# Kernel tuning notes

Measured on AMD Instinct MI355X. Metric: run time of the kernel, lower is better.

## Reference

```python
import jax, jax.numpy as jnp
import numpy as np

NEG_SLOPE = 0.01  # LeakyReLU default
STRIDE = 5        # group_length // 4
EPS = 1e-5        # RMSNorm eps


def leaky_relu(x):
    return jnp.where(x >= 0, x, NEG_SLOPE * x)


def rmsnorm(x, w):
    return x * jax.lax.rsqrt(jnp.mean(x * x, axis=-1, keepdims=True) + EPS) * w


def s6(x, fc1_w, fc1_b, fc2_w, fc2_b, fc3_w, fc3_b, A):
    # x: [B, L, D] with D = 2*d_model; A: [D, N]
    delta = jax.nn.softplus(x @ fc1_w.T + fc1_b)        # [B, L, D]
    Bm = x @ fc2_w.T + fc2_b                             # [B, L, N]
    Cm = x @ fc3_w.T + fc3_b                             # [B, L, N]
    dA = jnp.exp(jnp.einsum('bld,dn->bldn', delta, A))   # [B, L, D, N]
    dBx = jnp.einsum('bld,bln,bld->bldn', delta, Bm, x)  # delta * B * x

    def step(h, inp):
        dA_t, dBx_t = inp
        h = dA_t * h + dBx_t
        return h, h

    B_, L, D, N = dA.shape
    h0 = jnp.zeros((B_, D, N), dtype=x.dtype)
    _, hs = jax.lax.scan(step, h0, (jnp.swapaxes(dA, 0, 1), jnp.swapaxes(dBx, 0, 1)))
    hs = jnp.swapaxes(hs, 0, 1)                          # [B, L, D, N]
    return jnp.einsum('bln,bldn->bld', Cm, hs)           # [B, L, D]


def setup_inputs() -> dict:
    key = jax.random.key(0)
    ks = iter(jax.random.split(key, 32))

    def rn(shape, scale=0.02):
        return scale * jax.random.normal(next(ks), shape, dtype=jnp.float32)

    B, band, gl, d, N, L = 256, 189, 20, 128, 128, 34
    di = 2 * d
    return {
        'x': jax.random.normal(next(ks), (B, 1, band), dtype=jnp.float32),
        'conv_w': rn((d, 1, gl)), 'conv_b': rn((d,)),
        'norm_w': jnp.ones((d,), jnp.float32),
        'inp_w': rn((di, d)), 'inp_b': rn((di,)),
        'seqconv_w': rn((L, L, 3)), 'seqconv_b': rn((L,)),
        'convlin_w': rn((di, di)), 'convlin_b': rn((di,)),
        'fc1_w': rn((di, di)), 'fc1_b': rn((di,)),
        'fc2_w': rn((N, di)), 'fc2_b': rn((N,)),
        'fc3_w': rn((N, di)), 'fc3_b': rn((N,)),
        'A': jnp.ones((di, N), jnp.float32) / jnp.sqrt(jnp.float32(N)),
        'D_w': rn((di, d)), 'D_b': rn((di,)),
        'out_w': rn((d, di)), 'out_b': rn((d,)),
        'fnn1_w': rn((64, L * d)), 'fnn1_b': rn((64,)),
        'fnn2_w': rn((32, 64)), 'fnn2_b': rn((32,)),
    }


def reference(x, conv_w, conv_b, norm_w, inp_w, inp_b, seqconv_w, seqconv_b,
              convlin_w, convlin_b, fc1_w, fc1_b, fc2_w, fc2_b, fc3_w, fc3_b,
              A, D_w, D_b, out_w, out_b, fnn1_w, fnn1_b, fnn2_w, fnn2_b):
    # group division: Conv1d(1, d, k=20, stride=5) + LeakyReLU
    g = jax.lax.conv_general_dilated(x, conv_w, (STRIDE,), [(0, 0)],
                                     dimension_numbers=('NCH', 'OIH', 'NCH'))
    g = leaky_relu(g + conv_b[None, :, None])            # [B, d, L]
    h = jnp.swapaxes(g, 1, 2)                            # [B, L, d]
    # Mamba block
    xn = rmsnorm(h, norm_w)
    xp = xn @ inp_w.T + inp_b                            # [B, L, 2d]
    # Conv1d(seq_len, seq_len, k=3, pad=1): seq axis L is the channel dim
    xc = jax.lax.conv_general_dilated(xp, seqconv_w, (1,), [(1, 1)],
                                      dimension_numbers=('NCH', 'OIH', 'NCH'))
    xc = jax.nn.silu(xc + seqconv_b[None, :, None])
    xc = xc @ convlin_w.T + convlin_b                    # [B, L, 2d]
    xs = s6(xc, fc1_w, fc1_b, fc2_w, fc2_b, fc3_w, fc3_b, A)
    y = jax.nn.silu(xs) * jax.nn.silu(xn @ D_w.T + D_b)  # gated
    y = y @ out_w.T + out_b                              # [B, L, d]
    # FNN head
    f = y.reshape(y.shape[0], -1)                        # [B, L*d]
    f = leaky_relu(f @ fnn1_w.T + fnn1_b)
    return f @ fnn2_w.T + fnn2_b                         # [B, 32]
```

## Files before the change

kernel.cpp:

```cpp
#include <hip/hip_runtime.h>
#include <math.h>


#define NB    256
#define LL    34
#define DD    128
#define DI    256
#define NN    128
#define MM    (NB*LL)

using u16 = unsigned short;
typedef __attribute__((ext_vector_type(8))) short short8;
typedef __attribute__((ext_vector_type(4))) float f32x4;

__device__ __forceinline__ float silu_f(float x)  { return x / (1.f + __expf(-x)); }
__device__ __forceinline__ float softplus_f(float x) {
    return fmaxf(x, 0.f) + __logf(1.f + __expf(-fabsf(x)));
}
__device__ __forceinline__ float leaky_f(float x) { return (x >= 0.f) ? x : 0.01f * x; }

__device__ __forceinline__ u16 f2bf(float x) {
    unsigned u = __float_as_uint(x);
    return (u16)((u + 0x7FFF + ((u >> 16) & 1)) >> 16);
}
__device__ __forceinline__ float bf2f(u16 h) {
    return __uint_as_float(((unsigned)h) << 16);
}
__device__ __forceinline__ void f2pair(float v, u16* h, u16* l) {
    u16 hh = f2bf(v);
    *h = hh;
    *l = f2bf(v - bf2f(hh));
}

__global__ __launch_bounds__(256)
void prep_conv_k(const float* __restrict__ x, const float* __restrict__ cw,
                 const float* __restrict__ cb, const float* __restrict__ nw,
                 u16* __restrict__ XNh, u16* __restrict__ XNl,
                 const float* __restrict__ inp_w, const float* __restrict__ D_w,
                 const float* __restrict__ fc1_w, const float* __restrict__ fc2_w,
                 const float* __restrict__ fc3_w, const float* __restrict__ convlin_w,
                 const float* __restrict__ out_w,
                 const float* __restrict__ inp_b, const float* __restrict__ D_b,
                 const float* __restrict__ fc1_b, const float* __restrict__ fc2_b,
                 const float* __restrict__ fc3_b,
                 const float* __restrict__ W1, const float* __restrict__ A,
                 u16* __restrict__ wc1h, u16* __restrict__ wc1l,
                 u16* __restrict__ wc3h, u16* __restrict__ wc3l,
                 u16* __restrict__ cvh,  u16* __restrict__ cvl,
                 u16* __restrict__ owh,  u16* __restrict__ owl,
                 float* __restrict__ bias1, float* __restrict__ bias3,
                 float* __restrict__ W1T, int* __restrict__ flag)
{
    const int bx  = blockIdx.x;
    const int tid = threadIdx.x;
    __shared__ float tile[64][65];
    __shared__ float wsum[4];

    if (bx < 4352) {
        const int row = tid >> 7;
        const int c   = tid & 127;
        const int bl  = bx * 2 + row;
        const int b   = bl / LL, l = bl % LL;
        const float* xr = x + (size_t)b * 189 + l * 5;
        float g = cb[c];
        #pragma unroll
        for (int k = 0; k < 20; k++) g = fmaf(xr[k], cw[c * 20 + k], g);
        g = leaky_f(g);

        float s = g * g;
        #pragma unroll
        for (int m = 32; m >= 1; m >>= 1) s += __shfl_xor(s, m);
        if ((tid & 63) == 0) wsum[tid >> 6] = s;
        __syncthreads();
        float mean = (wsum[row * 2] + wsum[row * 2 + 1]) * (1.f / 128.f);
        float inv = 1.f / sqrtf(mean + 1e-5f);
        float v = g * inv * nw[c];
        f2pair(v, &XNh[(size_t)bl * DD + c], &XNl[(size_t)bl * DD + c]);
    } else if (bx < 5504) {
        int i = (bx - 4352) * 256 + tid;
        if (i < 65536) {
            float v = (i < 32768) ? inp_w[i] : D_w[i - 32768];
            f2pair(v, &wc1h[i], &wc1l[i]);
        } else if (i < 196608) {
            int j = i - 65536;
            float v = (j < 65536) ? fc1_w[j] : (j < 98304 ? fc2_w[j - 65536] : fc3_w[j - 98304]);
            f2pair(v, &wc3h[j], &wc3l[j]);
        } else if (i < 262144) {
            int j = i - 196608;
            f2pair(convlin_w[j], &cvh[j], &cvl[j]);
        } else if (i < 294912) {
            int j = i - 262144;
            f2pair(out_w[j], &owh[j], &owl[j]);
        }
        if (i < 512)  bias1[i] = (i < 256) ? inp_b[i] : D_b[i - 256];
        else if (i < 1024) {
            int j = i - 512;
            bias3[j] = (j < 256) ? fc1_b[j] : (j < 384 ? fc2_b[j - 256] : fc3_b[j - 384]);
        }
    } else if (bx < 5572) {
        const int bt = bx - 5504;
        for (int p = 0; p < 16; p++) {
            int idx = tid + p * 256;
            int r = idx >> 6, c = idx & 63;
            tile[r][c] = W1[(size_t)r * 4352 + bt * 64 + c];
        }
        __syncthreads();
        for (int p = 0; p < 16; p++) {
            int idx = tid + p * 256;
            int cc = idx >> 6, rr = idx & 63;
            W1T[(size_t)(bt * 64 + cc) * 64 + rr] = tile[rr][cc];
        }
    } else {
        __shared__ int s;
        if (tid == 0) s = 1;
        __syncthreads();
        bool ok = true;
        for (int k = 0; k < 128; k++) {
            int idx = tid + k * 256;
            ok &= (A[idx] == A[idx & ~127]);
        }
        if (!ok) s = 0;
        __syncthreads();
        if (tid == 0) *flag = s;
    }
}

template <int K, int EPI>
__global__ __launch_bounds__(256)
void mgemm_k(const u16* __restrict__ Ah, const u16* __restrict__ Al,
             const u16* __restrict__ Wh, const u16* __restrict__ Wl,
             const float* __restrict__ bias,
             float* __restrict__ Y, int ldy,
             u16* __restrict__ Yh, u16* __restrict__ Yl,
             u16* __restrict__ BC)
{
    const int tid  = threadIdx.x;
    const int r0   = blockIdx.x * 128;
    const int c0   = blockIdx.y * 64;
    const int wave = tid >> 6;
    const int lane = tid & 63;
    const int wm   = wave & 1;
    const int wn   = wave >> 1;
    const int l15  = lane & 15;
    const int lq   = lane >> 4;

    __shared__ u16 sAh[128][40];
    __shared__ u16 sAl[128][40];
    __shared__ u16 sBh[64][40];
    __shared__ u16 sBl[64][40];

    f32x4 acc[4][2];
    #pragma unroll
    for (int i = 0; i < 4; i++)
        #pragma unroll
        for (int j = 0; j < 2; j++) acc[i][j] = (f32x4){0.f, 0.f, 0.f, 0.f};

    const int a_row = tid >> 1;
    const int a_kb  = (tid & 1) * 16;
    const int b_row = tid >> 2;
    const int b_ko  = (tid & 3) * 8;

    for (int k0 = 0; k0 < K; k0 += 32) {
        const u16* ga = Ah + (size_t)(r0 + a_row) * K + k0 + a_kb;
        const u16* gl = Al + (size_t)(r0 + a_row) * K + k0 + a_kb;
        short8 vh0 = *(const short8*)(ga);
        short8 vh1 = *(const short8*)(ga + 8);
        short8 vl0 = *(const short8*)(gl);
        short8 vl1 = *(const short8*)(gl + 8);
        const u16* gb = Wh + (size_t)(c0 + b_row) * K + k0 + b_ko;
        const u16* gc = Wl + (size_t)(c0 + b_row) * K + k0 + b_ko;
        short8 wb = *(const short8*)(gb);
        short8 wc = *(const short8*)(gc);

        *(short8*)&sAh[a_row][a_kb]     = vh0;
        *(short8*)&sAh[a_row][a_kb + 8] = vh1;
        *(short8*)&sAl[a_row][a_kb]     = vl0;
        *(short8*)&sAl[a_row][a_kb + 8] = vl1;
        *(short8*)&sBh[b_row][b_ko] = wb;
        *(short8*)&sBl[b_row][b_ko] = wc;
        __syncthreads();

        short8 fah[4], fal[4], fbh[2], fbl[2];
        #pragma unroll
        for (int i = 0; i < 4; i++) {
            fah[i] = *(const short8*)&sAh[wm * 64 + i * 16 + l15][lq * 8];
            fal[i] = *(const short8*)&sAl[wm * 64 + i * 16 + l15][lq * 8];
        }
        #pragma unroll
        for (int j = 0; j < 2; j++) {
            fbh[j] = *(const short8*)&sBh[wn * 32 + j * 16 + l15][lq * 8];
            fbl[j] = *(const short8*)&sBl[wn * 32 + j * 16 + l15][lq * 8];
        }
        #pragma unroll
        for (int i = 0; i < 4; i++)
            #pragma unroll
            for (int j = 0; j < 2; j++) {
                acc[i][j] = __builtin_amdgcn_mfma_f32_16x16x32_bf16(fah[i], fbh[j], acc[i][j], 0, 0, 0);
                acc[i][j] = __builtin_amdgcn_mfma_f32_16x16x32_bf16(fah[i], fbl[j], acc[i][j], 0, 0, 0);
                acc[i][j] = __builtin_amdgcn_mfma_f32_16x16x32_bf16(fal[i], fbh[j], acc[i][j], 0, 0, 0);
            }
        __syncthreads();
    }

    #pragma unroll
    for (int i = 0; i < 4; i++) {
        int gr = r0 + wm * 64 + i * 16 + lq * 4;
        #pragma unroll
        for (int j = 0; j < 2; j++) {
            int gc = c0 + wn * 32 + j * 16 + l15;
            float bb = bias[gc];
            #pragma unroll
            for (int r = 0; r < 4; r++) {
                float v = acc[i][j][r] + bb;
                if (EPI == 1 || EPI == 3) { if (gc < 256) v = softplus_f(v); }
                if (EPI == 2) {
                    u16 hh, ll;
                    f2pair(v, &hh, &ll);
                    Yh[(size_t)(gr + r) * ldy + gc] = hh;
                    Yl[(size_t)(gr + r) * ldy + gc] = ll;
                } else {
                    Y[(size_t)(gr + r) * ldy + gc] = v;
                    if (EPI == 3 && gc >= 256) {
                        u16 hh, ll;
                        f2pair(v, &hh, &ll);
                        u16* rb = BC + (size_t)(gr + r) * 1024
                                     + ((gc < 384) ? 0 : 256) + (gc & 127);
                        rb[0]   = hh;
                        rb[128] = ll;
                    }
                }
            }
        }
    }
}

__global__ __launch_bounds__(256)
void seqconv_k(const float* __restrict__ XP, int ldxp,
               const float* __restrict__ w, const float* __restrict__ bias,
               u16* __restrict__ XCh, u16* __restrict__ XCl)
{
    const int b   = blockIdx.x;
    const int tid = threadIdx.x;
    const int tx  = tid & 63;
    const int ty  = tid >> 6;
    const int j0  = tx * 4;

    __shared__ float sx[LL][264];
    __shared__ float sw[LL][112];

    for (int idx = tid; idx < LL * 256; idx += 256) {
        int li = idx >> 8, jj = idx & 255;
        sx[li][jj + 1] = XP[(size_t)(b * LL + li) * ldxp + jj];
    }
    if (tid < LL) { sx[tid][0] = 0.f; sx[tid][257] = 0.f; }
    for (int idx = tid; idx < LL * LL * 3; idx += 256) {
        int lo = idx / 102;
        int rem = idx - lo * 102;
        int li = rem / 3;
        int k  = rem - li * 3;
        sw[li][lo * 3 + k] = w[idx];
    }
    __syncthreads();

    const int base = ty * 9 - (ty == 3 ? 1 : 0);
    const int cnt  = (ty < 2) ? 9 : 8;

    float acc[9][4];
    #pragma unroll
    for (int i = 0; i < 9; i++)
        #pragma unroll
        for (int jj = 0; jj < 4; jj++) acc[i][jj] = 0.f;

    for (int li = 0; li < LL; li++) {
        float4 xa = *(const float4*)&sx[li][j0];
        float2 xb = *(const float2*)&sx[li][j0 + 4];
        float xv[6] = {xa.x, xa.y, xa.z, xa.w, xb.x, xb.y};
        const float* swr = &sw[li][0];
        #pragma unroll
        for (int i = 0; i < 9; i++) {
            if (i < cnt) {
                int lo3 = (base + i) * 3;
                float w0 = swr[lo3 + 0];
                float w1 = swr[lo3 + 1];
                float w2 = swr[lo3 + 2];
                #pragma unroll
                for (int jj = 0; jj < 4; jj++) {
                    acc[i][jj] = fmaf(w0, xv[jj],     acc[i][jj]);
                    acc[i][jj] = fmaf(w1, xv[jj + 1], acc[i][jj]);
                    acc[i][jj] = fmaf(w2, xv[jj + 2], acc[i][jj]);
                }
            }
        }
    }

    #pragma unroll
    for (int i = 0; i < 9; i++) {
        if (i < cnt) {
            int lo = base + i;
            float bb = bias[lo];
            ushort4 oh, ol;
            float v0 = silu_f(acc[i][0] + bb);
            float v1 = silu_f(acc[i][1] + bb);
            float v2 = silu_f(acc[i][2] + bb);
            float v3 = silu_f(acc[i][3] + bb);
            f2pair(v0, &oh.x, &ol.x);
            f2pair(v1, &oh.y, &ol.y);
            f2pair(v2, &oh.z, &ol.z);
            f2pair(v3, &oh.w, &ol.w);
            size_t o = (size_t)(b * LL + lo) * DI + j0;
            *(ushort4*)&XCh[o] = oh;
            *(ushort4*)&XCl[o] = ol;
        }
    }
}

__global__ __launch_bounds__(256)
void scan_fb_k(const int* __restrict__ flag,
               const float* __restrict__ dBC,
               const u16*  __restrict__ Xh, const u16* __restrict__ Xl,
               const float* __restrict__ A,
               const float* __restrict__ DG,
               u16* __restrict__ Gh, u16* __restrict__ Gl)
{
    if (*flag != 0) return;
    const int b  = blockIdx.y;
    const int d0 = blockIdx.x * 64;
    const int tid = threadIdx.x;
    const int sub = tid & 15;
    const int pg  = tid >> 4;
    const int dbase = d0 + pg * 4;
    const int nA = sub * 4;

    float a[4][8], h[4][8];
    #pragma unroll
    for (int dd = 0; dd < 4; dd++) {
        const float* Ar = A + (size_t)(dbase + dd) * NN;
        float4 q0 = *(const float4*)(Ar + nA);
        float4 q1 = *(const float4*)(Ar + 64 + nA);
        a[dd][0]=q0.x; a[dd][1]=q0.y; a[dd][2]=q0.z; a[dd][3]=q0.w;
        a[dd][4]=q1.x; a[dd][5]=q1.y; a[dd][6]=q1.z; a[dd][7]=q1.w;
        #pragma unroll
        for (int j = 0; j < 8; j++) h[dd][j] = 0.f;
    }

    const float* pD  = dBC + (size_t)b * LL * 512 + dbase;
    const float* pBC = dBC + (size_t)b * LL * 512 + 256 + nA;
    const u16*  pXh = Xh  + (size_t)b * LL * 256 + dbase;
    const u16*  pXl = Xl  + (size_t)b * LL * 256 + dbase;
    const float* pG  = DG  + (size_t)b * LL * 512 + 256 + dbase;
    u16* pGh = Gh + (size_t)b * LL * 256 + dbase;
    u16* pGl = Gl + (size_t)b * LL * 256 + dbase;

    for (int l = 0; l < LL; l++) {
        float4  cD  = *(const float4*)(pD);
        ushort4 cXh = *(const ushort4*)(pXh);
        ushort4 cXl = *(const ushort4*)(pXl);
        float4 cB0 = *(const float4*)(pBC);
        float4 cB1 = *(const float4*)(pBC + 64);
        float4 cC0 = *(const float4*)(pBC + 128);
        float4 cC1 = *(const float4*)(pBC + 192);
        pD += 512; pBC += 512; pXh += 256; pXl += 256;

        float xv[4] = { bf2f(cXh.x) + bf2f(cXl.x), bf2f(cXh.y) + bf2f(cXl.y),
                        bf2f(cXh.z) + bf2f(cXl.z), bf2f(cXh.w) + bf2f(cXl.w) };
        float dl[4] = {cD.x, cD.y, cD.z, cD.w};
        float dx[4] = {cD.x * xv[0], cD.y * xv[1], cD.z * xv[2], cD.w * xv[3]};
        float bv[8] = {cB0.x,cB0.y,cB0.z,cB0.w,cB1.x,cB1.y,cB1.z,cB1.w};
        float cv[8] = {cC0.x,cC0.y,cC0.z,cC0.w,cC1.x,cC1.y,cC1.z,cC1.w};

        float accd[4] = {0.f, 0.f, 0.f, 0.f};
        #pragma unroll
        for (int dd = 0; dd < 4; dd++)
            #pragma unroll
            for (int j = 0; j < 8; j++) {
                float dA = __expf(dl[dd] * a[dd][j]);
                h[dd][j] = fmaf(dA, h[dd][j], dx[dd] * bv[j]);
                accd[dd] = fmaf(cv[j], h[dd][j], accd[dd]);
            }
        #pragma unroll
        for (int dd = 0; dd < 4; dd++) {
            float v = accd[dd];
            v += __shfl_xor(v, 1);
            v += __shfl_xor(v, 2);
            v += __shfl_xor(v, 4);
            v += __shfl_xor(v, 8);
            accd[dd] = v;
        }
        if (sub == 0) {
            float4 dg = *(const float4*)(pG);
            ushort4 oh, ol;
            float g0 = silu_f(accd[0]) * silu_f(dg.x);
            float g1 = silu_f(accd[1]) * silu_f(dg.y);
            float g2 = silu_f(accd[2]) * silu_f(dg.z);
            float g3 = silu_f(accd[3]) * silu_f(dg.w);
            f2pair(g0, &oh.x, &ol.x);
            f2pair(g1, &oh.y, &ol.y);
            f2pair(g2, &oh.z, &ol.z);
            f2pair(g3, &oh.w, &ol.w);
            *(ushort4*)pGh = oh;
            *(ushort4*)pGl = ol;
        }
        pG += 512; pGh += 256; pGl += 256;
    }
}

__global__ __launch_bounds__(512)
void ssd_tail_k(const int* __restrict__ flag,
                const float* __restrict__ dBC,
                const u16* __restrict__ BCp,
                const u16* __restrict__ Xh, const u16* __restrict__ Xl,
                const float* __restrict__ A,
                const float* __restrict__ DG,
                const u16* __restrict__ gFh, const u16* __restrict__ gFl,
                const u16* __restrict__ owh, const u16* __restrict__ owl,
                const float* __restrict__ outb,
                const float* __restrict__ W1T, const float* __restrict__ B1,
                const float* __restrict__ W2, const float* __restrict__ B2,
                float* __restrict__ out)
{
    const int b    = blockIdx.x;
    const int tid  = threadIdx.x;
    const int wave = tid >> 6;
    const int lane = tid & 63;
    const int l15  = lane & 15;
    const int lq   = lane >> 4;

    __shared__ __align__(16) char smem[71936];
    u16  (*sBh)[136] = (u16 (*)[136])(smem);
    u16  (*sBl)[136] = (u16 (*)[136])(smem + 13056);
    u16  (*sCh)[136] = (u16 (*)[136])(smem + 26112);
    u16  (*sCl)[136] = (u16 (*)[136])(smem + 39168);
    float (*sM)[49]  = (float (*)[49])(smem + 52224);
    u16  (*sGh)[264] = (u16 (*)[264])(smem);
    u16  (*sGl)[264] = (u16 (*)[264])(smem + 25344);
    float* sF        = (float*)(smem + 52224);
    float* s1p       = (float*)(smem + 69632);
    float* s1        = (float*)(smem + 71680);

    const bool uni = (*flag != 0);
    if (uni) {
        const u16* base = BCp + (size_t)b * LL * 1024;
        for (int idx = tid; idx < LL * 16; idx += 512) {
            int l = idx >> 4, c = (idx & 15) << 3;
            const u16* row = base + l * 1024;
            *(short8*)&sBh[l][c] = *(const short8*)&row[c];
            *(short8*)&sBl[l][c] = *(const short8*)&row[128 + c];
            *(short8*)&sCh[l][c] = *(const short8*)&row[256 + c];
            *(short8*)&sCl[l][c] = *(const short8*)&row[384 + c];
        }
        __syncthreads();

        for (int tt = wave; tt < 9; tt += 8) {
            int ti = tt / 3, tj = tt - ti * 3;
            f32x4 acc = (f32x4){0.f, 0.f, 0.f, 0.f};
            #pragma unroll
            for (int ks = 0; ks < 4; ks++) {
                short8 ch = *(const short8*)&sCh[ti * 16 + l15][ks * 32 + lq * 8];
                short8 cl = *(const short8*)&sCl[ti * 16 + l15][ks * 32 + lq * 8];
                short8 bh = *(const short8*)&sBh[tj * 16 + l15][ks * 32 + lq * 8];
                short8 bl = *(const short8*)&sBl[tj * 16 + l15][ks * 32 + lq * 8];
                acc = __builtin_amdgcn_mfma_f32_16x16x32_bf16(ch, bh, acc, 0, 0, 0);
                acc = __builtin_amdgcn_mfma_f32_16x16x32_bf16(ch, bl, acc, 0, 0, 0);
                acc = __builtin_amdgcn_mfma_f32_16x16x32_bf16(cl, bh, acc, 0, 0, 0);
            }
            #pragma unroll
            for (int r = 0; r < 4; r++)
                sM[ti * 16 + lq * 4 + r][tj * 16 + l15] = acc[r];
        }
        __syncthreads();

        if (tid < 256) {
            const int d = tid;
            const float a_d = A[(size_t)d * NN];
            const float* pDel = dBC + (size_t)b * LL * 512 + d;
            const u16* pXh = Xh + (size_t)b * LL * 256 + d;
            const u16* pXl = Xl + (size_t)b * LL * 256 + d;

            float u[LL], eS[LL];
            float S = 0.f;
            #pragma unroll
            for (int l = 0; l < LL; l++) {
                float dl = pDel[l * 512];
                S = fmaf(dl, a_d, S);
                eS[l] = __expf(S);
                float xv = bf2f(pXh[l * 256]) + bf2f(pXl[l * 256]);
                u[l] = __expf(-S) * dl * xv;
            }

            const float* pG = DG + (size_t)b * LL * 512 + 256 + d;
            #pragma unroll
            for (int l = 0; l < LL; l++) {
                float acc = 0.f;
                for (int t = 0; t <= l; t++) acc = fmaf(sM[l][t], u[t], acc);
                float xs = eS[l] * acc;
                float g = silu_f(xs) * silu_f(pG[l * 512]);
                u16 hh, ll2;
                f2pair(g, &hh, &ll2);
                sGh[l][d] = hh;
                sGl[l][d] = ll2;
            }
        } else {
            u16* zh = &sGh[34][0];
            u16* zl = &sGl[34][0];
            for (int idx = tid - 256; idx < 14 * 264; idx += 256) {
                zh[idx] = 0;
                zl[idx] = 0;
            }
        }
        __syncthreads();
    } else {
        for (int idx = tid; idx < LL * 32; idx += 512) {
            int l = idx >> 5, c = (idx & 31) << 3;
            *(short8*)&sGh[l][c] = *(const short8*)&gFh[((size_t)b * LL + l) * 256 + c];
            *(short8*)&sGl[l][c] = *(const short8*)&gFl[((size_t)b * LL + l) * 256 + c];
        }
        u16* zh = &sGh[34][0];
        u16* zl = &sGl[34][0];
        for (int idx = tid; idx < 14 * 264; idx += 512) {
            zh[idx] = 0;
            zl[idx] = 0;
        }
        __syncthreads();
    }

    {
        const int j0 = wave;
        f32x4 acc[3];
        #pragma unroll
        for (int i = 0; i < 3; i++) acc[i] = (f32x4){0.f, 0.f, 0.f, 0.f};
        #pragma unroll
        for (int ks = 0; ks < 8; ks++) {
            const size_t wo = (size_t)(j0 * 16 + l15) * 256 + ks * 32 + lq * 8;
            short8 bh = *(const short8*)&owh[wo];
            short8 bl = *(const short8*)&owl[wo];
            #pragma unroll
            for (int i = 0; i < 3; i++) {
                short8 ah = *(const short8*)&sGh[i * 16 + l15][ks * 32 + lq * 8];
                short8 al = *(const short8*)&sGl[i * 16 + l15][ks * 32 + lq * 8];
                acc[i] = __builtin_amdgcn_mfma_f32_16x16x32_bf16(ah, bh, acc[i], 0, 0, 0);
                acc[i] = __builtin_amdgcn_mfma_f32_16x16x32_bf16(ah, bl, acc[i], 0, 0, 0);
                acc[i] = __builtin_amdgcn_mfma_f32_16x16x32_bf16(al, bh, acc[i], 0, 0, 0);
            }
        }
        __syncthreads();
        #pragma unroll
        for (int i = 0; i < 3; i++) {
            int row = i * 16 + lq * 4;
            int col = j0 * 16 + l15;
            float bb = outb[col];
            #pragma unroll
            for (int r = 0; r < 4; r++)
                if (row + r < LL) sF[(row + r) * 128 + col] = acc[i][r] + bb;
        }
    }
    __syncthreads();

    {
        const int o = tid & 63;
        const int q = tid >> 6;
        const float* wp = W1T + ((size_t)q * 544) * 64 + o;
        const float* fp = sF + q * 544;
        float accf = 0.f;
        for (int k = 0; k < 544; k += 4) {
            float w0 = wp[(size_t)(k + 0) * 64];
            float w1 = wp[(size_t)(k + 1) * 64];
            float w2 = wp[(size_t)(k + 2) * 64];
            float w3 = wp[(size_t)(k + 3) * 64];
            accf = fmaf(w0, fp[k + 0], accf);
            accf = fmaf(w1, fp[k + 1], accf);
            accf = fmaf(w2, fp[k + 2], accf);
            accf = fmaf(w3, fp[k + 3], accf);
        }
        s1p[q * 64 + o] = accf;
    }
    __syncthreads();

    if (tid < 64) {
        float a0 = B1[tid];
        #pragma unroll
        for (int q = 0; q < 8; q++) a0 += s1p[q * 64 + tid];
        s1[tid] = leaky_f(a0);
    }
    __syncthreads();

    if (tid < 32) {
        float a2 = B2[tid];
        const float* w2 = W2 + tid * 64;
        #pragma unroll
        for (int j = 0; j < 64; j++) a2 = fmaf(s1[j], w2[j], a2);
        out[(size_t)b * 32 + tid] = a2;
    }
}

extern "C" void kernel_launch(void* const* d_in, const int* in_sizes, int n_in,
                              void* d_out, int out_size, void* d_ws, size_t ws_size,
                              hipStream_t stream)
{
    const float* x        = (const float*)d_in[0];
    const float* conv_w   = (const float*)d_in[1];
    const float* conv_b   = (const float*)d_in[2];
    const float* norm_w   = (const float*)d_in[3];
    const float* inp_w    = (const float*)d_in[4];
    const float* inp_b    = (const float*)d_in[5];
    const float* seqconv_w= (const float*)d_in[6];
    const float* seqconv_b= (const float*)d_in[7];
    const float* convlin_w= (const float*)d_in[8];
    const float* convlin_b= (const float*)d_in[9];
    const float* fc1_w    = (const float*)d_in[10];
    const float* fc1_b    = (const float*)d_in[11];
    const float* fc2_w    = (const float*)d_in[12];
    const float* fc2_b    = (const float*)d_in[13];
    const float* fc3_w    = (const float*)d_in[14];
    const float* fc3_b    = (const float*)d_in[15];
    const float* A        = (const float*)d_in[16];
    const float* D_w      = (const float*)d_in[17];
    const float* D_b      = (const float*)d_in[18];
    const float* out_w    = (const float*)d_in[19];
    const float* out_b    = (const float*)d_in[20];
    const float* fnn1_w   = (const float*)d_in[21];
    const float* fnn1_b   = (const float*)d_in[22];
    const float* fnn2_w   = (const float*)d_in[23];
    const float* fnn2_b   = (const float*)d_in[24];

    char* W = (char*)d_ws;
    float* buf1  = (float*)(W + 0);
    float* buf3  = (float*)(W + 17825792);
    u16*   xnh   = (u16*)  (W + 35651584);
    u16*   xnl   = (u16*)  (W + 37879808);
    u16*   xc2h  = (u16*)  (W + 35651584);
    u16*   xc2l  = (u16*)  (W + 40108032);
    u16*   xch   = (u16*)  (W + 44564480);
    u16*   xcl   = (u16*)  (W + 49020928);
    float* w1t   = (float*)(W + 53477376);
    u16*   wc1h  = (u16*)  (W + 54591488);
    u16*   wc1l  = (u16*)  (W + 54722560);
    u16*   wc3h  = (u16*)  (W + 54853632);
    u16*   wc3l  = (u16*)  (W + 55115776);
    u16*   cvh   = (u16*)  (W + 55377920);
    u16*   cvl   = (u16*)  (W + 55508992);
    u16*   owh   = (u16*)  (W + 55640064);
    u16*   owl   = (u16*)  (W + 55705600);
    float* bias1 = (float*)(W + 55771136);
    float* bias3 = (float*)(W + 55773184);
    int*   uflag = (int*)  (W + 55775232);
    u16* gateh = xch;
    u16* gatel = xcl;
    u16* bcpair = (u16*)buf1;

    prep_conv_k<<<5573, 256, 0, stream>>>(x, conv_w, conv_b, norm_w, xnh, xnl,
                                          inp_w, D_w, fc1_w, fc2_w, fc3_w,
                                          convlin_w, out_w,
                                          inp_b, D_b, fc1_b, fc2_b, fc3_b,
                                          fnn1_w, A,
                                          wc1h, wc1l, wc3h, wc3l, cvh, cvl,
                                          owh, owl, bias1, bias3, w1t, uflag);

    mgemm_k<128, 0><<<dim3(MM / 128, 8), 256, 0, stream>>>(
        xnh, xnl, wc1h, wc1l, bias1, buf1, 512, nullptr, nullptr, nullptr);

    seqconv_k<<<NB, 256, 0, stream>>>(buf1, 512, seqconv_w, seqconv_b, xch, xcl);

    mgemm_k<256, 2><<<dim3(MM / 128, 4), 256, 0, stream>>>(
        xch, xcl, cvh, cvl, convlin_b, nullptr, 256, xc2h, xc2l, nullptr);

    mgemm_k<256, 3><<<dim3(MM / 128, 8), 256, 0, stream>>>(
        xc2h, xc2l, wc3h, wc3l, bias3, buf3, 512, nullptr, nullptr, bcpair);

    scan_fb_k<<<dim3(4, NB), 256, 0, stream>>>(uflag, buf3, xc2h, xc2l, A,
                                               buf1, gateh, gatel);

    ssd_tail_k<<<NB, 512, 0, stream>>>(uflag, buf3, bcpair, xc2h, xc2l, A,
                                       buf1, gateh, gatel, owh, owl, out_b,
                                       w1t, fnn1_b, fnn2_w, fnn2_b,
                                       (float*)d_out);
}
```

Baseline: 210.9 us.

## Fuse seqconv, convlin, fc GEMM and SSD tail into per-batch megakernel

Replaces the seqconv kernel, two full-size GEMM launches and the SSD tail with one per-batch kernel. It keeps the seqconv output, convlin output and B/C projections in shared memory, then runs the uniform-A SSD path and the out projection in place, writing an fp32 feature matrix. The FNN head moves to separate split-K kernels that tile across batches to reuse the fnn1 weights. The aim is to cut global round-trips and launch count. The cost is 256 blocks of 512 threads using about 107KB LDS each, which limits occupancy, plus weights reloaded per block from global and an extra pair of head launches.

After: 201.9 us. -4.3%, faster.

```diff
diff --git a/kernel.cpp b/kernel.cpp
--- a/kernel.cpp
+++ b/kernel.cpp
@@ -234,82 +234,321 @@
     }
 }
 
-__global__ __launch_bounds__(256)
-void seqconv_k(const float* __restrict__ XP, int ldxp,
-               const float* __restrict__ w, const float* __restrict__ bias,
-               u16* __restrict__ XCh, u16* __restrict__ XCl)
+__global__ __launch_bounds__(512)
+void mega2_k(const int* __restrict__ flag,
+             const float* __restrict__ buf1,
+             const float* __restrict__ scw, const float* __restrict__ scb,
+             const u16* __restrict__ cvh, const u16* __restrict__ cvl,
+             const float* __restrict__ clb,
+             const u16* __restrict__ wc3h, const u16* __restrict__ wc3l,
+             const float* __restrict__ bias3,
+             const float* __restrict__ A,
+             const u16* __restrict__ owh, const u16* __restrict__ owl,
+             const float* __restrict__ outb,
+             float* __restrict__ buf3,
+             u16* __restrict__ bcpair,
+             u16* __restrict__ xc2h, u16* __restrict__ xc2l,
+             float* __restrict__ fout)
 {
-    const int b   = blockIdx.x;
-    const int tid = threadIdx.x;
-    const int tx  = tid & 63;
-    const int ty  = tid >> 6;
-    const int j0  = tx * 4;
-
-    __shared__ float sx[LL][264];
-    __shared__ float sw[LL][112];
-
-    for (int idx = tid; idx < LL * 256; idx += 256) {
+    const int b    = blockIdx.x;
+    const int tid  = threadIdx.x;
+    const int wave = tid >> 6;
+    const int lane = tid & 63;
+    const int l15  = lane & 15;
+    const int lq   = lane >> 4;
+
+    __shared__ __align__(16) char smem[109584];
+    float (*sx)[264] = (float (*)[264])(smem);
+    float (*sw)[112] = (float (*)[112])(smem + 35904);
+    u16 (*sXch)[264] = (u16 (*)[264])(smem);
+    u16 (*sXcl)[264] = (u16 (*)[264])(smem + 25344);
+    u16 (*sBh)[136]  = (u16 (*)[136])(smem);
+    u16 (*sBl)[136]  = (u16 (*)[136])(smem + 13056);
+    u16 (*sCh)[136]  = (u16 (*)[136])(smem + 26112);
+    u16 (*sCl)[136]  = (u16 (*)[136])(smem + 39168);
+    u16 (*sGh)[264]  = (u16 (*)[264])(smem);
+    u16 (*sGl)[264]  = (u16 (*)[264])(smem + 25344);
+    u16 (*sX2h)[264] = (u16 (*)[264])(smem + 52224);
+    u16 (*sX2l)[264] = (u16 (*)[264])(smem + 77568);
+    float (*sM)[49]  = (float (*)[49])(smem + 102912);
+
+    const bool uni = (*flag != 0);
+
+    for (int idx = tid; idx < LL * 256; idx += 512) {
         int li = idx >> 8, jj = idx & 255;
-        sx[li][jj + 1] = XP[(size_t)(b * LL + li) * ldxp + jj];
+        sx[li][jj + 1] = buf1[(size_t)(b * LL + li) * 512 + jj];
     }
     if (tid < LL) { sx[tid][0] = 0.f; sx[tid][257] = 0.f; }
-    for (int idx = tid; idx < LL * LL * 3; idx += 256) {
+    for (int idx = tid; idx < LL * LL * 3; idx += 512) {
         int lo = idx / 102;
         int rem = idx - lo * 102;
         int li = rem / 3;
         int k  = rem - li * 3;
-        sw[li][lo * 3 + k] = w[idx];
+        sw[li][lo * 3 + k] = scw[idx];
     }
     __syncthreads();
 
-    const int base = ty * 9 - (ty == 3 ? 1 : 0);
-    const int cnt  = (ty < 2) ? 9 : 8;
-
-    float acc[9][4];
-    #pragma unroll
-    for (int i = 0; i < 9; i++)
-        #pragma unroll
-        for (int jj = 0; jj < 4; jj++) acc[i][jj] = 0.f;
-
-    for (int li = 0; li < LL; li++) {
-        float4 xa = *(const float4*)&sx[li][j0];
-        float2 xb = *(const float2*)&sx[li][j0 + 4];
-        float xv[6] = {xa.x, xa.y, xa.z, xa.w, xb.x, xb.y};
-        const float* swr = &sw[li][0];
-        #pragma unroll
-        for (int i = 0; i < 9; i++) {
-            if (i < cnt) {
-                int lo3 = (base + i) * 3;
-                float w0 = swr[lo3 + 0];
-                float w1 = swr[lo3 + 1];
-                float w2 = swr[lo3 + 2];
+    {
+        const int tx  = tid & 63;
+        const int ty  = tid >> 6;
+        const int j0c = tx * 4;
+        const int cbase = (ty < 2) ? ty * 5 : 10 + (ty - 2) * 4;
+        const int ccnt  = (ty < 2) ? 5 : 4;
+
+        float cacc[5][4];
+        #pragma unroll
+        for (int i = 0; i < 5; i++)
+            #pragma unroll
+            for (int jj = 0; jj < 4; jj++) cacc[i][jj] = 0.f;
+
+        for (int li = 0; li < LL; li++) {
+            float4 xa = *(const float4*)&sx[li][j0c];
+            float2 xb = *(const float2*)&sx[li][j0c + 4];
+            float xv[6] = {xa.x, xa.y, xa.z, xa.w, xb.x, xb.y};
+            const float* swr = &sw[li][0];
+            #pragma unroll
+            for (int i = 0; i < 5; i++) {
+                if (i < ccnt) {
+                    int lo3 = (cbase + i) * 3;
+                    float w0 = swr[lo3 + 0];
+                    float w1 = swr[lo3 + 1];
+                    float w2 = swr[lo3 + 2];
+                    #pragma unroll
+                    for (int jj = 0; jj < 4; jj++) {
+                        cacc[i][jj] = fmaf(w0, xv[jj],     cacc[i][jj]);
+                        cacc[i][jj] = fmaf(w1, xv[jj + 1], cacc[i][jj]);
+                        cacc[i][jj] = fmaf(w2, xv[jj + 2], cacc[i][jj]);
+                    }
+                }
+            }
+        }
+        __syncthreads();
+
+        #pragma unroll
+        for (int i = 0; i < 5; i++) {
+            if (i < ccnt) {
+                int lo = cbase + i;
+                float bb = scb[lo];
+                ushort4 oh, ol;
+                float v0 = silu_f(cacc[i][0] + bb);
+                float v1 = silu_f(cacc[i][1] + bb);
+                float v2 = silu_f(cacc[i][2] + bb);
+                float v3 = silu_f(cacc[i][3] + bb);
+                f2pair(v0, &oh.x, &ol.x);
+                f2pair(v1, &oh.y, &ol.y);
+                f2pair(v2, &oh.z, &ol.z);
+                f2pair(v3, &oh.w, &ol.w);
+                *(ushort4*)&sXch[lo][j0c] = oh;
+                *(ushort4*)&sXcl[lo][j0c] = ol;
+            }
+        }
+    }
+    __syncthreads();
+
+    {
+        const int c0 = wave * 32;
+        f32x4 a2[3][2];
+        #pragma unroll
+        for (int i = 0; i < 3; i++)
+            #pragma unroll
+            for (int j = 0; j < 2; j++) a2[i][j] = (f32x4){0.f, 0.f, 0.f, 0.f};
+
+        #pragma unroll
+        for (int ks = 0; ks < 8; ks++) {
+            short8 fh[3], fl[3];
+            #pragma unroll
+            for (int i = 0; i < 3; i++) {
+                fh[i] = *(const short8*)&sXch[i * 16 + l15][ks * 32 + lq * 8];
+                fl[i] = *(const short8*)&sXcl[i * 16 + l15][ks * 32 + lq * 8];
+            }
+            #pragma unroll
+            for (int j = 0; j < 2; j++) {
+                const size_t wo = (size_t)(c0 + j * 16 + l15) * 256 + ks * 32 + lq * 8;
+                short8 bh = *(const short8*)&cvh[wo];
+                short8 bl = *(const short8*)&cvl[wo];
                 #pragma unroll
-                for (int jj = 0; jj < 4; jj++) {
-                    acc[i][jj] = fmaf(w0, xv[jj],     acc[i][jj]);
-                    acc[i][jj] = fmaf(w1, xv[jj + 1], acc[i][jj]);
-                    acc[i][jj] = fmaf(w2, xv[jj + 2], acc[i][jj]);
+                for (int i = 0; i < 3; i++) {
+                    a2[i][j] = __builtin_amdgcn_mfma_f32_16x16x32_bf16(fh[i], bh, a2[i][j], 0, 0, 0);
+                    a2[i][j] = __builtin_amdgcn_mfma_f32_16x16x32_bf16(fh[i], bl, a2[i][j], 0, 0, 0);
+                    a2[i][j] = __builtin_amdgcn_mfma_f32_16x16x32_bf16(fl[i], bh, a2[i][j], 0, 0, 0);
                 }
             }
         }
-    }
-
-    #pragma unroll
-    for (int i = 0; i < 9; i++) {
-        if (i < cnt) {
-            int lo = base + i;
-            float bb = bias[lo];
-            ushort4 oh, ol;
-            float v0 = silu_f(acc[i][0] + bb);
-            float v1 = silu_f(acc[i][1] + bb);
-            float v2 = silu_f(acc[i][2] + bb);
-            float v3 = silu_f(acc[i][3] + bb);
-            f2pair(v0, &oh.x, &ol.x);
-            f2pair(v1, &oh.y, &ol.y);
-            f2pair(v2, &oh.z, &ol.z);
-            f2pair(v3, &oh.w, &ol.w);
-            size_t o = (size_t)(b * LL + lo) * DI + j0;
-            *(ushort4*)&XCh[o] = oh;
-            *(ushort4*)&XCl[o] = ol;
+        #pragma unroll
+        for (int i = 0; i < 3; i++) {
+            int row = i * 16 + lq * 4;
+            #pragma unroll
+            for (int j = 0; j < 2; j++) {
+                int col = c0 + j * 16 + l15;
+                float bb = clb[col];
+                #pragma unroll
+                for (int r = 0; r < 4; r++) {
+                    float v = a2[i][j][r] + bb;
+                    u16 hh, ll;
+                    f2pair(v, &hh, &ll);
+                    sX2h[row + r][col] = hh;
+                    sX2l[row + r][col] = ll;
+                    if (!uni && (row + r) < LL) {
+                        xc2h[(size_t)(b * LL + row + r) * 256 + col] = hh;
+                        xc2l[(size_t)(b * LL + row + r) * 256 + col] = ll;
+                    }
+                }
+            }
+        }
+    }
+    __syncthreads();
+
+    {
+        const int c0 = wave * 64;
+        f32x4 a3[3][4];
+        #pragma unroll
+        for (int i = 0; i < 3; i++)
+            #pragma unroll
+            for (int j = 0; j < 4; j++) a3[i][j] = (f32x4){0.f, 0.f, 0.f, 0.f};
+
+        #pragma unroll
+        for (int ks = 0; ks < 8; ks++) {
+            short8 fh[3], fl[3];
+            #pragma unroll
+            for (int i = 0; i < 3; i++) {
+                fh[i] = *(const short8*)&sX2h[i * 16 + l15][ks * 32 + lq * 8];
+                fl[i] = *(const short8*)&sX2l[i * 16 + l15][ks * 32 + lq * 8];
+            }
+            #pragma unroll
+            for (int j = 0; j < 4; j++) {
+                const size_t wo = (size_t)(c0 + j * 16 + l15) * 256 + ks * 32 + lq * 8;
+                short8 bh = *(const short8*)&wc3h[wo];
+                short8 bl = *(const short8*)&wc3l[wo];
+                #pragma unroll
+                for (int i = 0; i < 3; i++) {
+                    a3[i][j] = __builtin_amdgcn_mfma_f32_16x16x32_bf16(fh[i], bh, a3[i][j], 0, 0, 0);
+                    a3[i][j] = __builtin_amdgcn_mfma_f32_16x16x32_bf16(fh[i], bl, a3[i][j], 0, 0, 0);
+                    a3[i][j] = __builtin_amdgcn_mfma_f32_16x16x32_bf16(fl[i], bh, a3[i][j], 0, 0, 0);
+                }
+            }
+        }
+        #pragma unroll
+        for (int i = 0; i < 3; i++) {
+            int row = i * 16 + lq * 4;
+            #pragma unroll
+            for (int j = 0; j < 4; j++) {
+                int col = c0 + j * 16 + l15;
+                float bb = bias3[col];
+                #pragma unroll
+                for (int r = 0; r < 4; r++) {
+                    float v = a3[i][j][r] + bb;
+                    int rr = row + r;
+                    if (col < 256) {
+                        v = softplus_f(v);
+                        if (rr < LL) buf3[((size_t)b * LL + rr) * 512 + col] = v;
+                    } else {
+                        u16 hh, ll;
+                        f2pair(v, &hh, &ll);
+                        int cc = col & 127;
+                        if (col < 384) { sBh[rr][cc] = hh; sBl[rr][cc] = ll; }
+                        else           { sCh[rr][cc] = hh; sCl[rr][cc] = ll; }
+                        if (!uni && rr < LL) {
+                            buf3[((size_t)b * LL + rr) * 512 + col] = v;
+                            u16* rb = bcpair + ((size_t)b * LL + rr) * 1024
+                                      + ((col < 384) ? 0 : 256) + cc;
+                            rb[0]   = hh;
+                            rb[128] = ll;
+                        }
+                    }
+                }
+            }
+        }
+    }
+    __syncthreads();
+    if (!uni) return;
+
+    for (int tt = wave; tt < 9; tt += 8) {
+        int ti = tt / 3, tj = tt - ti * 3;
+        f32x4 acc = (f32x4){0.f, 0.f, 0.f, 0.f};
+        #pragma unroll
+        for (int ks = 0; ks < 4; ks++) {
+            short8 ch = *(const short8*)&sCh[ti * 16 + l15][ks * 32 + lq * 8];
+            short8 cl = *(const short8*)&sCl[ti * 16 + l15][ks * 32 + lq * 8];
+            short8 bh = *(const short8*)&sBh[tj * 16 + l15][ks * 32 + lq * 8];
+            short8 bl = *(const short8*)&sBl[tj * 16 + l15][ks * 32 + lq * 8];
+            acc = __builtin_amdgcn_mfma_f32_16x16x32_bf16(ch, bh, acc, 0, 0, 0);
+            acc = __builtin_amdgcn_mfma_f32_16x16x32_bf16(ch, bl, acc, 0, 0, 0);
+            acc = __builtin_amdgcn_mfma_f32_16x16x32_bf16(cl, bh, acc, 0, 0, 0);
+        }
+        #pragma unroll
+        for (int r = 0; r < 4; r++) {
+            int row = ti * 16 + lq * 4 + r;
+            if (row < LL) sM[row][tj * 16 + l15] = acc[r];
+        }
+    }
+    __syncthreads();
+
+    if (tid < 256) {
+        const int d = tid;
+        const float a_d = A[(size_t)d * NN];
+        const float* pDel = buf3 + (size_t)b * LL * 512 + d;
+
+        float u[LL], eS[LL];
+        float S = 0.f;
+        #pragma unroll
+        for (int l = 0; l < LL; l++) {
+            float dl = pDel[l * 512];
+            S = fmaf(dl, a_d, S);
+            eS[l] = __expf(S);
+            float xv = bf2f(sX2h[l][d]) + bf2f(sX2l[l][d]);
+            u[l] = __expf(-S) * dl * xv;
+        }
+
+        const float* pG = buf1 + (size_t)b * LL * 512 + 256 + d;
+        #pragma unroll
+        for (int l = 0; l < LL; l++) {
+            float acc = 0.f;
+            for (int t = 0; t <= l; t++) acc = fmaf(sM[l][t], u[t], acc);
+            float xs = eS[l] * acc;
+            float g = silu_f(xs) * silu_f(pG[l * 512]);
+            u16 hh, ll2;
+            f2pair(g, &hh, &ll2);
+            sGh[l][d] = hh;
+            sGl[l][d] = ll2;
+        }
+    } else {
+        u16* zh = &sGh[34][0];
+        u16* zl = &sGl[34][0];
+        for (int idx = tid - 256; idx < 14 * 264; idx += 256) {
+            zh[idx] = 0;
+            zl[idx] = 0;
+        }
+    }
+    __syncthreads();
+
+    {
+        const int j0 = wave;
+        f32x4 a4[3];
+        #pragma unroll
+        for (int i = 0; i < 3; i++) a4[i] = (f32x4){0.f, 0.f, 0.f, 0.f};
+        #pragma unroll
+        for (int ks = 0; ks < 8; ks++) {
+            const size_t wo = (size_t)(j0 * 16 + l15) * 256 + ks * 32 + lq * 8;
+            short8 bh = *(const short8*)&owh[wo];
+            short8 bl = *(const short8*)&owl[wo];
+            #pragma unroll
+            for (int i = 0; i < 3; i++) {
+                short8 ah = *(const short8*)&sGh[i * 16 + l15][ks * 32 + lq * 8];
+                short8 al = *(const short8*)&sGl[i * 16 + l15][ks * 32 + lq * 8];
+                a4[i] = __builtin_amdgcn_mfma_f32_16x16x32_bf16(ah, bh, a4[i], 0, 0, 0);
+                a4[i] = __builtin_amdgcn_mfma_f32_16x16x32_bf16(ah, bl, a4[i], 0, 0, 0);
+                a4[i] = __builtin_amdgcn_mfma_f32_16x16x32_bf16(al, bh, a4[i], 0, 0, 0);
+            }
+        }
+        #pragma unroll
+        for (int i = 0; i < 3; i++) {
+            int row = i * 16 + lq * 4;
+            int col = j0 * 16 + l15;
+            float bb = outb[col];
+            #pragma unroll
+            for (int r = 0; r < 4; r++)
+                if (row + r < LL)
+                    fout[(size_t)(b * LL + row + r) * 128 + col] = a4[i][r] + bb;
         }
     }
 }
@@ -405,19 +644,13 @@
 }
 
 __global__ __launch_bounds__(512)
-void ssd_tail_k(const int* __restrict__ flag,
-                const float* __restrict__ dBC,
-                const u16* __restrict__ BCp,
-                const u16* __restrict__ Xh, const u16* __restrict__ Xl,
-                const float* __restrict__ A,
-                const float* __restrict__ DG,
-                const u16* __restrict__ gFh, const u16* __restrict__ gFl,
-                const u16* __restrict__ owh, const u16* __restrict__ owl,
-                const float* __restrict__ outb,
-                const float* __restrict__ W1T, const float* __restrict__ B1,
-                const float* __restrict__ W2, const float* __restrict__ B2,
-                float* __restrict__ out)
+void tail_cold_k(const int* __restrict__ flag,
+                 const u16* __restrict__ gFh, const u16* __restrict__ gFl,
+                 const u16* __restrict__ owh, const u16* __restrict__ owl,
+                 const float* __restrict__ outb,
+                 float* __restrict__ fout)
 {
+    if (*flag != 0) return;
     const int b    = blockIdx.x;
     const int tid  = threadIdx.x;
     const int wave = tid >> 6;
@@ -425,170 +658,113 @@
     const int l15  = lane & 15;
     const int lq   = lane >> 4;
 
-    __shared__ __align__(16) char smem[71936];
-    u16  (*sBh)[136] = (u16 (*)[136])(smem);
-    u16  (*sBl)[136] = (u16 (*)[136])(smem + 13056);
-    u16  (*sCh)[136] = (u16 (*)[136])(smem + 26112);
-    u16  (*sCl)[136] = (u16 (*)[136])(smem + 39168);
-    float (*sM)[49]  = (float (*)[49])(smem + 52224);
-    u16  (*sGh)[264] = (u16 (*)[264])(smem);
-    u16  (*sGl)[264] = (u16 (*)[264])(smem + 25344);
-    float* sF        = (float*)(smem + 52224);
-    float* s1p       = (float*)(smem + 69632);
-    float* s1        = (float*)(smem + 71680);
-
-    const bool uni = (*flag != 0);
-    if (uni) {
-        const u16* base = BCp + (size_t)b * LL * 1024;
-        for (int idx = tid; idx < LL * 16; idx += 512) {
-            int l = idx >> 4, c = (idx & 15) << 3;
-            const u16* row = base + l * 1024;
-            *(short8*)&sBh[l][c] = *(const short8*)&row[c];
-            *(short8*)&sBl[l][c] = *(const short8*)&row[128 + c];
-            *(short8*)&sCh[l][c] = *(const short8*)&row[256 + c];
-            *(short8*)&sCl[l][c] = *(const short8*)&row[384 + c];
-        }
-        __syncthreads();
-
-        for (int tt = wave; tt < 9; tt += 8) {
-            int ti = tt / 3, tj = tt - ti * 3;
-            f32x4 acc = (f32x4){0.f, 0.f, 0.f, 0.f};
-            #pragma unroll
-            for (int ks = 0; ks < 4; ks++) {
-                short8 ch = *(const short8*)&sCh[ti * 16 + l15][ks * 32 + lq * 8];
-                short8 cl = *(const short8*)&sCl[ti * 16 + l15][ks * 32 + lq * 8];
-                short8 bh = *(const short8*)&sBh[tj * 16 + l15][ks * 32 + lq * 8];
-                short8 bl = *(const short8*)&sBl[tj * 16 + l15][ks * 32 + lq * 8];
-                acc = __builtin_amdgcn_mfma_f32_16x16x32_bf16(ch, bh, acc, 0, 0, 0);
-                acc = __builtin_amdgcn_mfma_f32_16x16x32_bf16(ch, bl, acc, 0, 0, 0);
-                acc = __builtin_amdgcn_mfma_f32_16x16x32_bf16(cl, bh, acc, 0, 0, 0);
-            }
-            #pragma unroll
-            for (int r = 0; r < 4; r++)
-                sM[ti * 16 + lq * 4 + r][tj * 16 + l15] = acc[r];
-        }
-        __syncthreads();
-
-        if (tid < 256) {
-            const int d = tid;
-            const float a_d = A[(size_t)d * NN];
-            const float* pDel = dBC + (size_t)b * LL * 512 + d;
-            const u16* pXh = Xh + (size_t)b * LL * 256 + d;
-            const u16* pXl = Xl + (size_t)b * LL * 256 + d;
-
-            float u[LL], eS[LL];
-            float S = 0.f;
-            #pragma unroll
-            for (int l = 0; l < LL; l++) {
-                float dl = pDel[l * 512];
-                S = fmaf(dl, a_d, S);
-                eS[l] = __expf(S);
-                float xv = bf2f(pXh[l * 256]) + bf2f(pXl[l * 256]);
-                u[l] = __expf(-S) * dl * xv;
-            }
-
-            const float* pG = DG + (size_t)b * LL * 512 + 256 + d;
-            #pragma unroll
-            for (int l = 0; l < LL; l++) {
-                float acc = 0.f;
-                for (int t = 0; t <= l; t++) acc = fmaf(sM[l][t], u[t], acc);
-                float xs = eS[l] * acc;
-                float g = silu_f(xs) * silu_f(pG[l * 512]);
-                u16 hh, ll2;
-                f2pair(g, &hh, &ll2);
-                sGh[l][d] = hh;
-                sGl[l][d] = ll2;
-            }
-        } else {
-            u16* zh = &sGh[34][0];
-            u16* zl = &sGl[34][0];
-            for (int idx = tid - 256; idx < 14 * 264; idx += 256) {
-                zh[idx] = 0;
-                zl[idx] = 0;
-            }
-        }
-        __syncthreads();
-    } else {
-        for (int idx = tid; idx < LL * 32; idx += 512) {
-            int l = idx >> 5, c = (idx & 31) << 3;
-            *(short8*)&sGh[l][c] = *(const short8*)&gFh[((size_t)b * LL + l) * 256 + c];
-            *(short8*)&sGl[l][c] = *(const short8*)&gFl[((size_t)b * LL + l) * 256 + c];
-        }
+    __shared__ u16 sGh[48][264];
+    __shared__ u16 sGl[48][264];
+
+    for (int idx = tid; idx < LL * 32; idx += 512) {
+        int l = idx >> 5, c = (idx & 31) << 3;
+        *(short8*)&sGh[l][c] = *(const short8*)&gFh[((size_t)b * LL + l) * 256 + c];
+        *(short8*)&sGl[l][c] = *(const short8*)&gFl[((size_t)b * LL + l) * 256 + c];
+    }
+    {
         u16* zh = &sGh[34][0];
         u16* zl = &sGl[34][0];
         for (int idx = tid; idx < 14 * 264; idx += 512) {
             zh[idx] = 0;
             zl[idx] = 0;
         }
-        __syncthreads();
-    }
-
-    {
-        const int j0 = wave;
-        f32x4 acc[3];
-        #pragma unroll
-        for (int i = 0; i < 3; i++) acc[i] = (f32x4){0.f, 0.f, 0.f, 0.f};
-        #pragma unroll
-        for (int ks = 0; ks < 8; ks++) {
-            const size_t wo = (size_t)(j0 * 16 + l15) * 256 + ks * 32 + lq * 8;
-            short8 bh = *(const short8*)&owh[wo];
-            short8 bl = *(const short8*)&owl[wo];
-            #pragma unroll
-            for (int i = 0; i < 3; i++) {
-                short8 ah = *(const short8*)&sGh[i * 16 + l15][ks * 32 + lq * 8];
-                short8 al = *(const short8*)&sGl[i * 16 + l15][ks * 32 + lq * 8];
-                acc[i] = __builtin_amdgcn_mfma_f32_16x16x32_bf16(ah, bh, acc[i], 0, 0, 0);
-                acc[i] = __builtin_amdgcn_mfma_f32_16x16x32_bf16(ah, bl, acc[i], 0, 0, 0);
-                acc[i] = __builtin_amdgcn_mfma_f32_16x16x32_bf16(al, bh, acc[i], 0, 0, 0);
-            }
-        }
-        __syncthreads();
+    }
+    __syncthreads();
+
+    const int j0 = wave;
+    f32x4 a4[3];
+    #pragma unroll
+    for (int i = 0; i < 3; i++) a4[i] = (f32x4){0.f, 0.f, 0.f, 0.f};
+    #pragma unroll
+    for (int ks = 0; ks < 8; ks++) {
+        const size_t wo = (size_t)(j0 * 16 + l15) * 256 + ks * 32 + lq * 8;
+        short8 bh = *(const short8*)&owh[wo];
+        short8 bl = *(const short8*)&owl[wo];
         #pragma unroll
         for (int i = 0; i < 3; i++) {
-            int row = i * 16 + lq * 4;
-            int col = j0 * 16 + l15;
-            float bb = outb[col];
-            #pragma unroll
-            for (int r = 0; r < 4; r++)
-                if (row + r < LL) sF[(row + r) * 128 + col] = acc[i][r] + bb;
-        }
+            short8 ah = *(const short8*)&sGh[i * 16 + l15][ks * 32 + lq * 8];
+            short8 al = *(const short8*)&sGl[i * 16 + l15][ks * 32 + lq * 8];
+            a4[i] = __builtin_amdgcn_mfma_f32_16x16x32_bf16(ah, bh, a4[i], 0, 0, 0);
+            a4[i] = __builtin_amdgcn_mfma_f32_16x16x32_bf16(ah, bl, a4[i], 0, 0, 0);
+            a4[i] = __builtin_amdgcn_mfma_f32_16x16x32_bf16(al, bh, a4[i], 0, 0, 0);
+        }
+    }
+    #pragma unroll
+    for (int i = 0; i < 3; i++) {
+        int row = i * 16 + lq * 4;
+        int col = j0 * 16 + l15;
+        float bb = outb[col];
+        #pragma unroll
+        for (int r = 0; r < 4; r++)
+            if (row + r < LL)
+                fout[(size_t)(b * LL + row + r) * 128 + col] = a4[i][r] + bb;
+    }
+}
+
+__global__ __launch_bounds__(256)
+void fnn1_k(const float* __restrict__ F, const float* __restrict__ W1T,
+            float* __restrict__ partials)
+{
+    const int btile = blockIdx.x;
+    const int kc    = blockIdx.y;
+    const int tid   = threadIdx.x;
+    __shared__ float sf[16][260];
+    for (int i = tid; i < 16 * 256; i += 256) {
+        int r = i >> 8, c = i & 255;
+        sf[r][c] = F[(size_t)(btile * 16 + r) * 4352 + kc * 256 + c];
     }
     __syncthreads();
 
-    {
-        const int o = tid & 63;
-        const int q = tid >> 6;
-        const float* wp = W1T + ((size_t)q * 544) * 64 + o;
-        const float* fp = sF + q * 544;
-        float accf = 0.f;
-        for (int k = 0; k < 544; k += 4) {
-            float w0 = wp[(size_t)(k + 0) * 64];
-            float w1 = wp[(size_t)(k + 1) * 64];
-            float w2 = wp[(size_t)(k + 2) * 64];
-            float w3 = wp[(size_t)(k + 3) * 64];
-            accf = fmaf(w0, fp[k + 0], accf);
-            accf = fmaf(w1, fp[k + 1], accf);
-            accf = fmaf(w2, fp[k + 2], accf);
-            accf = fmaf(w3, fp[k + 3], accf);
-        }
-        s1p[q * 64 + o] = accf;
-    }
+    const int o  = tid & 63;
+    const int bq = tid >> 6;
+    const float* w = W1T + (size_t)(kc * 256) * 64 + o;
+    float acc[4] = {0.f, 0.f, 0.f, 0.f};
+    for (int k = 0; k < 256; k += 4) {
+        float w0 = w[(size_t)(k + 0) * 64];
+        float w1 = w[(size_t)(k + 1) * 64];
+        float w2 = w[(size_t)(k + 2) * 64];
+        float w3 = w[(size_t)(k + 3) * 64];
+        #pragma unroll
+        for (int bj = 0; bj < 4; bj++) {
+            float4 f4 = *(const float4*)&sf[bq * 4 + bj][k];
+            acc[bj] = fmaf(w0, f4.x, acc[bj]);
+            acc[bj] = fmaf(w1, f4.y, acc[bj]);
+            acc[bj] = fmaf(w2, f4.z, acc[bj]);
+            acc[bj] = fmaf(w3, f4.w, acc[bj]);
+        }
+    }
+    #pragma unroll
+    for (int bj = 0; bj < 4; bj++)
+        partials[(size_t)kc * 16384 + (btile * 16 + bq * 4 + bj) * 64 + o] = acc[bj];
+}
+
+__global__ __launch_bounds__(64)
+void fnn2_k(const float* __restrict__ partials,
+            const float* __restrict__ B1,
+            const float* __restrict__ W2, const float* __restrict__ B2,
+            float* __restrict__ out)
+{
+    int b = blockIdx.x;
+    int t = threadIdx.x;
+    __shared__ float s1[64];
+    float acc = B1[t];
+    #pragma unroll
+    for (int kc = 0; kc < 17; kc++)
+        acc += partials[(size_t)kc * 16384 + b * 64 + t];
+    s1[t] = leaky_f(acc);
     __syncthreads();
 
-    if (tid < 64) {
-        float a0 = B1[tid];
-        #pragma unroll
-        for (int q = 0; q < 8; q++) a0 += s1p[q * 64 + tid];
-        s1[tid] = leaky_f(a0);
-    }
-    __syncthreads();
-
-    if (tid < 32) {
-        float a2 = B2[tid];
-        const float* w2 = W2 + tid * 64;
-        #pragma unroll
-        for (int j = 0; j < 64; j++) a2 = fmaf(s1[j], w2[j], a2);
-        out[(size_t)b * 32 + tid] = a2;
+    if (t < 32) {
+        float acc2 = B2[t];
+        const float* w2 = W2 + t * 64;
+        #pragma unroll
+        for (int j = 0; j < 64; j++) acc2 = fmaf(s1[j], w2[j], acc2);
+        out[(size_t)b * 32 + t] = acc2;
     }
 }
 
@@ -628,9 +804,10 @@
     u16*   xnh   = (u16*)  (W + 35651584);
     u16*   xnl   = (u16*)  (W + 37879808);
     u16*   xc2h  = (u16*)  (W + 35651584);
+    float* fout  = (float*)(W + 35651584);
     u16*   xc2l  = (u16*)  (W + 40108032);
-    u16*   xch   = (u16*)  (W + 44564480);
-    u16*   xcl   = (u16*)  (W + 49020928);
+    u16*   gateh = (u16*)  (W + 44564480);
+    u16*   gatel = (u16*)  (W + 49020928);
     float* w1t   = (float*)(W + 53477376);
     u16*   wc1h  = (u16*)  (W + 54591488);
     u16*   wc1l  = (u16*)  (W + 54722560);
@@ -643,9 +820,8 @@
     float* bias1 = (float*)(W + 55771136);
     float* bias3 = (float*)(W + 55773184);
     int*   uflag = (int*)  (W + 55775232);
-    u16* gateh = xch;
-    u16* gatel = xcl;
     u16* bcpair = (u16*)buf1;
+    float* partials = buf3;
 
     prep_conv_k<<<5573, 256, 0, stream>>>(x, conv_w, conv_b, norm_w, xnh, xnl,
                                           inp_w, D_w, fc1_w, fc2_w, fc3_w,
@@ -658,19 +834,17 @@
     mgemm_k<128, 0><<<dim3(MM / 128, 8), 256, 0, stream>>>(
         xnh, xnl, wc1h, wc1l, bias1, buf1, 512, nullptr, nullptr, nullptr);
 
-    seqconv_k<<<NB, 256, 0, stream>>>(buf1, 512, seqconv_w, seqconv_b, xch, xcl);
-
-    mgemm_k<256, 2><<<dim3(MM / 128, 4), 256, 0, stream>>>(
-        xch, xcl, cvh, cvl, convlin_b, nullptr, 256, xc2h, xc2l, nullptr);
-
-    mgemm_k<256, 3><<<dim3(MM / 128, 8), 256, 0, stream>>>(
-        xc2h, xc2l, wc3h, wc3l, bias3, buf3, 512, nullptr, nullptr, bcpair);
+    mega2_k<<<NB, 512, 0, stream>>>(uflag, buf1, seqconv_w, seqconv_b,
+                                    cvh, cvl, convlin_b, wc3h, wc3l, bias3,
+                                    A, owh, owl, out_b,
+                                    buf3, bcpair, xc2h, xc2l, fout);
 
     scan_fb_k<<<dim3(4, NB), 256, 0, stream>>>(uflag, buf3, xc2h, xc2l, A,
                                                buf1, gateh, gatel);
-
-    ssd_tail_k<<<NB, 512, 0, stream>>>(uflag, buf3, bcpair, xc2h, xc2l, A,
-                                       buf1, gateh, gatel, owh, owl, out_b,
-                                       w1t, fnn1_b, fnn2_w, fnn2_b,
-                                       (float*)d_out);
-}
+    tail_cold_k<<<NB, 512, 0, stream>>>(uflag, gateh, gatel, owh, owl, out_b,
+                                        fout);
+
+    fnn1_k<<<dim3(16, 17), 256, 0, stream>>>(fout, w1t, partials);
+    fnn2_k<<<NB, 64, 0, stream>>>(partials, fnn1_b, fnn2_w, fnn2_b,
+                                  (float*)d_out);
+}
```
